# Optimization experiments

Measured on AMD Instinct MI355X. Metric: run time of the kernel, lower is better.

The kernel has to match this reference:

```python
import jax, jax.numpy as jnp
import numpy as np

B = 4096        # batch_size (world_size = 1)
D = 128         # embedding dim
TEMP = 0.5      # temperature
EPS = 1e-8      # torch CosineSimilarity eps
BIG = 1e9       # diagonal masking constant


def setup_inputs() -> dict:
    key = jax.random.key(0)
    k1, k2 = jax.random.split(key)
    z_i = jax.random.normal(k1, (B, D), dtype=jnp.float32)
    z_j = jax.random.normal(k2, (B, D), dtype=jnp.float32)
    return {"z_i": z_i, "z_j": z_j}


def reference(z_i, z_j):
    N = 2 * B
    z = jnp.concatenate([z_i, z_j], axis=0)                    # [N, D]
    # cosine similarity: normalize once, then a single GEMM (avoids NxNxD)
    norm = jnp.maximum(jnp.linalg.norm(z, axis=1, keepdims=True), EPS)
    zn = z / norm                                              # [N, D]
    sim = (zn @ zn.T) / TEMP                                   # [N, N]
    # mask self-similarity on the diagonal
    sim = sim - BIG * jnp.eye(N, dtype=sim.dtype)
    # positive of row i is i+B (first half) or i-B (second half)
    labels = jnp.concatenate([jnp.arange(B) + B, jnp.arange(B)])  # [N]
    # cross-entropy, reduction='sum', then divide by N
    logp = jax.nn.log_softmax(sim, axis=1)                     # [N, N]
    loss = -jnp.sum(jnp.take_along_axis(logp, labels[:, None], axis=1)) / N
    return loss
```

## Files before the change

kernel.cpp:

```cpp
#include <hip/hip_runtime.h>
#include <hip/hip_bf16.h>
#include <hip/hip_fp16.h>

#define NB   4096
#define NTOT 8192
#define DD   128
#define ROWB 256
#define NCHUNK 32

typedef __attribute__((ext_vector_type(8))) _Float16 f16x8;
typedef __attribute__((ext_vector_type(4))) float    f32x4;

#if defined(__has_builtin)
#if __has_builtin(__builtin_amdgcn_exp2f)
#define EXP2F(x) __builtin_amdgcn_exp2f(x)
#else
#define EXP2F(x) exp2f(x)
#endif
#if __has_builtin(__builtin_amdgcn_logf)
#define LOG2F(x) __builtin_amdgcn_logf(x)
#else
#define LOG2F(x) log2f(x)
#endif
#else
#define EXP2F(x) exp2f(x)
#define LOG2F(x) log2f(x)
#endif

#define SQSCALE 1.69864394f
#define LN2     0.69314718056f


__global__ void knorm(const float* __restrict__ zi, const float* __restrict__ zj,
                      _Float16* __restrict__ zs, float* __restrict__ out) {
  int wave = threadIdx.x >> 6, lane = threadIdx.x & 63;
  int j = lane & 31;
  int row = (blockIdx.x << 3) + (wave << 1) + (lane >> 5);
  const float* src = (row < NB) ? (zi + (size_t)row * DD)
                                : (zj + (size_t)(row - NB) * DD);
  float4 v = ((const float4*)src)[j];
  float ss = v.x * v.x + v.y * v.y + v.z * v.z + v.w * v.w;
#pragma unroll
  for (int m = 1; m < 32; m <<= 1) ss += __shfl_xor(ss, m, 64);
  float inv = SQSCALE / fmaxf(sqrtf(ss), 1e-8f);
  struct H4 { _Float16 a, b, c, d; } hv;
  hv.a = (_Float16)(v.x * inv); hv.b = (_Float16)(v.y * inv);
  hv.c = (_Float16)(v.z * inv); hv.d = (_Float16)(v.w * inv);
  int phys = (j >> 1) ^ (row & 15);
  char* dst = (char*)zs + (size_t)row * ROWB + phys * 16 + (j & 1) * 8;
  *(uint2*)dst = __builtin_bit_cast(uint2, hv);
  if (blockIdx.x == 0 && threadIdx.x == 0) out[0] = 0.f;
}

__device__ __forceinline__ void gl_lds16(const char* g, char* l) {
  __builtin_amdgcn_global_load_lds(
      (const __attribute__((address_space(1))) void*)g,
      (__attribute__((address_space(3))) void*)l, 16, 0, 0);
}

__global__ __launch_bounds__(256) void kmain(const _Float16* __restrict__ zs,
                                             float* __restrict__ partial,
                                             float* __restrict__ slabel) {
  __shared__ f16x8 sB[2][1024];
  int rb    = blockIdx.x >> 5;
  int chunk = blockIdx.x & 31;
  int wave  = threadIdx.x >> 6;
  int lane  = threadIdx.x & 63;
  int q = lane >> 4;
  int c = lane & 15;
  int d = c - (q << 2);
  int rowbase = rb * 128 + wave * 32;
  int colchunk = chunk * 256;

  f16x8 a[2][4];
#pragma unroll
  for (int st = 0; st < 2; st++) {
    const char* p = (const char*)zs + (size_t)(rowbase + st * 16 + c) * ROWB;
#pragma unroll
    for (int kk = 0; kk < 4; kk++)
      a[st][kk] = *(const f16x8*)(p + (((kk << 2) + q) ^ c) * 16);
  }

  float part[2][4] = {{0.f, 0.f, 0.f, 0.f}, {0.f, 0.f, 0.f, 0.f}};

  const char* gB = (const char*)zs + (size_t)colchunk * ROWB;
  int soff = wave * 4096 + lane * 16;

  auto stage = [&](int s) {
    const char* g = gB + (size_t)s * (64 * ROWB) + soff;
    char* l = (char*)&sB[s & 1][0] + soff;
    gl_lds16(g, l);
    gl_lds16(g + 1024, l + 1024);
    gl_lds16(g + 2048, l + 2048);
    gl_lds16(g + 3072, l + 3072);
  };

  auto compute = [&](int s) {
    const char* base = (const char*)&sB[s & 1][0];
#pragma unroll
    for (int t = 0; t < 4; t++) {
      int colbase = colchunk + s * 64 + t * 16;
      f16x8 b[4];
      const char* bp = base + (t * 16 + c) * ROWB;
#pragma unroll
      for (int kk = 0; kk < 4; kk++)
        b[kk] = *(const f16x8*)(bp + (((kk << 2) + q) ^ c) * 16);
#pragma unroll
      for (int st = 0; st < 2; st++) {
        int sbase = rowbase + st * 16;
        f32x4 acc = {0.f, 0.f, 0.f, 0.f};
#pragma unroll
        for (int kk = 0; kk < 4; kk++)
          acc = __builtin_amdgcn_mfma_f32_16x16x32_f16(a[st][kk], b[kk], acc, 0, 0, 0);
        if (colbase == (sbase ^ NB)) {
#pragma unroll
          for (int r = 0; r < 4; r++)
            if (d == r) slabel[sbase + c] = acc[r];
        }
        if (colbase == sbase) {
#pragma unroll
          for (int r = 0; r < 4; r++)
            part[st][r] += (d == r) ? 0.f : EXP2F(acc[r]);
        } else {
#pragma unroll
          for (int r = 0; r < 4; r++)
            part[st][r] += EXP2F(acc[r]);
        }
      }
    }
  };

  stage(0);
  __syncthreads();
  for (int s = 0; s < 4; s++) {
    if (s + 1 < 4) stage(s + 1);
    compute(s);
    __syncthreads();
  }

  float* ebuf = (float*)&sB[0][0];
#pragma unroll
  for (int st = 0; st < 2; st++)
#pragma unroll
    for (int r = 0; r < 4; r++) {
      float v = part[st][r];
      v += __shfl_xor(v, 1, 64);
      v += __shfl_xor(v, 2, 64);
      v += __shfl_xor(v, 4, 64);
      v += __shfl_xor(v, 8, 64);
      if (c == 0) ebuf[wave * 32 + st * 16 + (q << 2) + r] = v;
    }
  __syncthreads();
  if (threadIdx.x < 128)
    partial[(size_t)chunk * NTOT + rb * 128 + threadIdx.x] = ebuf[threadIdx.x];
}

__global__ void kfinal(const float* __restrict__ partial,
                       const float* __restrict__ slabel,
                       float* __restrict__ out) {
  int i = blockIdx.x * 256 + threadIdx.x;
  float s = 0.f;
#pragma unroll
  for (int k = 0; k < NCHUNK; k++) s += partial[(size_t)k * NTOT + i];
  float acc = LN2 * (LOG2F(s) - slabel[i]);
#pragma unroll
  for (int m = 1; m < 64; m <<= 1) acc += __shfl_xor(acc, m, 64);
  __shared__ float wsum[4];
  int tid = threadIdx.x;
  if ((tid & 63) == 0) wsum[tid >> 6] = acc;
  __syncthreads();
  if (tid == 0)
    atomicAdd(out, (wsum[0] + wsum[1] + wsum[2] + wsum[3]) * (1.0f / (float)NTOT));
}

extern "C" void kernel_launch(void* const* d_in, const int* in_sizes, int n_in,
                              void* d_out, int out_size, void* d_ws, size_t ws_size,
                              hipStream_t stream) {
  const float* zi = (const float*)d_in[0];
  const float* zj = (const float*)d_in[1];
  float* out = (float*)d_out;

  char* ws = (char*)d_ws;
  const size_t ZS_BYTES = (size_t)NTOT * DD * sizeof(_Float16);
  _Float16* zs   = (_Float16*)ws;
  float* partial = (float*)(ws + ZS_BYTES);
  float* slabel  = (float*)(ws + ZS_BYTES + (size_t)NCHUNK * NTOT * 4);

  knorm<<<NTOT / 8, 256, 0, stream>>>(zi, zj, zs, out);
  kmain<<<(NTOT / 128) * NCHUNK, 256, 0, stream>>>(zs, partial, slabel);
  kfinal<<<NTOT / 256, 256, 0, stream>>>(partial, slabel, out);
}
```

Measured before the change: 89.79 us.

## Exploit symmetry of similarity matrix to compute only upper-triangular tiles

```diff
diff --git a/kernel.cpp b/kernel.cpp
--- a/kernel.cpp
+++ b/kernel.cpp
@@ -6,7 +6,7 @@
 #define NTOT 8192
 #define DD   128
 #define ROWB 256
-#define NCHUNK 32
+#define NSLOT 64
 
 typedef __attribute__((ext_vector_type(8))) _Float16 f16x8;
 typedef __attribute__((ext_vector_type(4))) float    f32x4;
@@ -61,16 +61,18 @@
 __global__ __launch_bounds__(256) void kmain(const _Float16* __restrict__ zs,
                                              float* __restrict__ partial,
                                              float* __restrict__ slabel) {
+  int rb = blockIdx.x >> 6;
+  int cb = blockIdx.x & 63;
+  if (cb < rb) return;
   __shared__ f16x8 sB[2][1024];
-  int rb    = blockIdx.x >> 5;
-  int chunk = blockIdx.x & 31;
   int wave  = threadIdx.x >> 6;
   int lane  = threadIdx.x & 63;
   int q = lane >> 4;
   int c = lane & 15;
   int d = c - (q << 2);
   int rowbase = rb * 128 + wave * 32;
-  int colchunk = chunk * 256;
+  int colchunk = cb * 128;
+  bool diagblk = (rb == cb);
 
   f16x8 a[2][4];
 #pragma unroll
@@ -81,7 +83,8 @@
       a[st][kk] = *(const f16x8*)(p + (((kk << 2) + q) ^ c) * 16);
   }
 
-  float part[2][4] = {{0.f, 0.f, 0.f, 0.f}, {0.f, 0.f, 0.f, 0.f}};
+  float part[2][4] = {{0.f,0.f,0.f,0.f},{0.f,0.f,0.f,0.f}};
+  float cpart[8] = {0,0,0,0,0,0,0,0};
 
   const char* gB = (const char*)zs + (size_t)colchunk * ROWB;
   int soff = wave * 4096 + lane * 16;
@@ -99,7 +102,8 @@
     const char* base = (const char*)&sB[s & 1][0];
 #pragma unroll
     for (int t = 0; t < 4; t++) {
-      int colbase = colchunk + s * 64 + t * 16;
+      int tt = s * 4 + t;
+      int colbase = colchunk + tt * 16;
       f16x8 b[4];
       const char* bp = base + (t * 16 + c) * ROWB;
 #pragma unroll
@@ -115,16 +119,25 @@
         if (colbase == (sbase ^ NB)) {
 #pragma unroll
           for (int r = 0; r < 4; r++)
-            if (d == r) slabel[sbase + c] = acc[r];
+            if (d == r) {
+              slabel[sbase + c] = acc[r];
+              slabel[(sbase + c) ^ NB] = acc[r];
+            }
         }
         if (colbase == sbase) {
 #pragma unroll
-          for (int r = 0; r < 4; r++)
-            part[st][r] += (d == r) ? 0.f : EXP2F(acc[r]);
+          for (int r = 0; r < 4; r++) {
+            float e = (d == r) ? 0.f : EXP2F(acc[r]);
+            part[st][r] += e;
+            cpart[tt]   += e;
+          }
         } else {
 #pragma unroll
-          for (int r = 0; r < 4; r++)
-            part[st][r] += EXP2F(acc[r]);
+          for (int r = 0; r < 4; r++) {
+            float e = EXP2F(acc[r]);
+            part[st][r] += e;
+            cpart[tt]   += e;
+          }
         }
       }
     }
@@ -132,13 +145,15 @@
 
   stage(0);
   __syncthreads();
-  for (int s = 0; s < 4; s++) {
-    if (s + 1 < 4) stage(s + 1);
+  for (int s = 0; s < 2; s++) {
+    if (s + 1 < 2) stage(s + 1);
     compute(s);
     __syncthreads();
   }
 
-  float* ebuf = (float*)&sB[0][0];
+  float* ebuf  = (float*)&sB[0][0];
+  float* cwave = ebuf + 128;
+
 #pragma unroll
   for (int st = 0; st < 2; st++)
 #pragma unroll
@@ -150,9 +165,23 @@
       v += __shfl_xor(v, 8, 64);
       if (c == 0) ebuf[wave * 32 + st * 16 + (q << 2) + r] = v;
     }
+  if (!diagblk) {
+#pragma unroll
+    for (int tt = 0; tt < 8; tt++) {
+      float v = cpart[tt];
+      v += __shfl_xor(v, 16, 64);
+      v += __shfl_xor(v, 32, 64);
+      if (q == 0) cwave[wave * 128 + tt * 16 + c] = v;
+    }
+  }
   __syncthreads();
-  if (threadIdx.x < 128)
-    partial[(size_t)chunk * NTOT + rb * 128 + threadIdx.x] = ebuf[threadIdx.x];
+  if (threadIdx.x < 128) {
+    partial[(size_t)cb * NTOT + rb * 128 + threadIdx.x] = ebuf[threadIdx.x];
+  } else if (!diagblk) {
+    int col = threadIdx.x - 128;
+    float s = cwave[col] + cwave[128 + col] + cwave[256 + col] + cwave[384 + col];
+    partial[(size_t)rb * NTOT + cb * 128 + col] = s;
+  }
 }
 
 __global__ void kfinal(const float* __restrict__ partial,
@@ -160,8 +189,8 @@
                        float* __restrict__ out) {
   int i = blockIdx.x * 256 + threadIdx.x;
   float s = 0.f;
-#pragma unroll
-  for (int k = 0; k < NCHUNK; k++) s += partial[(size_t)k * NTOT + i];
+#pragma unroll 8
+  for (int k = 0; k < NSLOT; k++) s += partial[(size_t)k * NTOT + i];
   float acc = LN2 * (LOG2F(s) - slabel[i]);
 #pragma unroll
   for (int m = 1; m < 64; m <<= 1) acc += __shfl_xor(acc, m, 64);
@@ -184,9 +213,9 @@
   const size_t ZS_BYTES = (size_t)NTOT * DD * sizeof(_Float16);
   _Float16* zs   = (_Float16*)ws;
   float* partial = (float*)(ws + ZS_BYTES);
-  float* slabel  = (float*)(ws + ZS_BYTES + (size_t)NCHUNK * NTOT * 4);
+  float* slabel  = (float*)(ws + ZS_BYTES + (size_t)NSLOT * NTOT * 4);
 
   knorm<<<NTOT / 8, 256, 0, stream>>>(zi, zj, zs, out);
-  kmain<<<(NTOT / 128) * NCHUNK, 256, 0, stream>>>(zs, partial, slabel);
+  kmain<<<64 * 64, 256, 0, stream>>>(zs, partial, slabel);
   kfinal<<<NTOT / 256, 256, 0, stream>>>(partial, slabel, out);
 }
```

New measurement: 89.10 us. About the same (-0.8%).
